# Kernel optimization log

Hardware: AMD Instinct MI355X
Metric: run time of the kernel (lower is better)

## Reference

```python
import jax, jax.numpy as jnp
import numpy as np

B, N, D = 8, 2048, 512
S = 4096  # max_swaps


def setup_inputs() -> dict:
    key = jax.random.key(0)
    ks = jax.random.split(key, 5)
    h = jax.random.normal(ks[0], (B, N, D), dtype=jnp.float32)
    indices = jax.random.randint(ks[1], (B, S, 4), 0, N, dtype=jnp.int64)
    # MLP params (Linear stores weight as (out,in) in torch; we keep (in,out) and matmul)
    W1 = jax.random.normal(ks[2], (4 * D, D), dtype=jnp.float32) * (1.0 / np.sqrt(4 * D))
    b1 = jnp.zeros((D,), dtype=jnp.float32)
    W2 = jax.random.normal(ks[3], (D, D // 2), dtype=jnp.float32) * (1.0 / np.sqrt(D))
    b2 = jnp.zeros((D // 2,), dtype=jnp.float32)
    W3 = jax.random.normal(ks[4], (D // 2, 1), dtype=jnp.float32) * (1.0 / np.sqrt(D // 2))
    b3 = jnp.zeros((1,), dtype=jnp.float32)
    return {"h": h, "indices": indices, "W1": W1, "b1": b1, "W2": W2, "b2": b2, "W3": W3, "b3": b3}


def reference(h, indices, W1, b1, W2, b2, W3, b3):
    # h: (B, N, D); indices: (B, S, 4) node ids per swap
    swap_emb = jnp.take_along_axis(h[:, None, :, :], indices[..., None].astype(jnp.int32),
                                   axis=2)  # broadcast-gather -> (B, S, 4, D)
    # equivalently: h[batch_idx, indices]; implemented as per-batch gather
    swap_emb = jax.vmap(lambda hb, ib: hb[ib])(h, indices)  # (B, S, 4, D)
    swap_feats = swap_emb.reshape(h.shape[0], indices.shape[1], -1)  # (B, S, 4D)
    x = jax.nn.gelu(swap_feats @ W1 + b1, approximate=False)
    x = jax.nn.gelu(x @ W2 + b2, approximate=False)
    scores = (x @ W3 + b3)[..., 0]  # (B, S)
    rates = jax.nn.softplus(scores)
    return rates
```

## Files before the change

kernel.cpp:

```cpp
#include <hip/hip_runtime.h>
#include <math.h>

#define BATCH 8
#define NNODES 2048
#define DDIM 512
#define SWAPS 4096
#define M_TOTAL (BATCH * SWAPS)
#define MD (BATCH * NNODES)
#define KD DDIM
#define ND (4 * DDIM)
#define K2 DDIM
#define N2 (DDIM / 2)

typedef __attribute__((ext_vector_type(8))) __bf16 bf16x8;
typedef __attribute__((ext_vector_type(4))) float f32x4;
typedef __attribute__((ext_vector_type(8))) unsigned short us8;
typedef unsigned short ushort_t;

__device__ __forceinline__ float gelu_exact(float x) {
    return 0.5f * x * (1.0f + erff(x * 0.70710678118654752440f));
}
__device__ __forceinline__ float softplus_f(float x) {
    return fmaxf(x, 0.0f) + log1pf(expf(-fabsf(x)));
}
__device__ __forceinline__ unsigned short f2bf(float f) {
    unsigned int u = __builtin_bit_cast(unsigned int, f);
    u += 0x7FFFu + ((u >> 16) & 1u);
    return (unsigned short)(u >> 16);
}
__device__ __forceinline__ float bf2f(unsigned short s) {
    return __builtin_bit_cast(float, (unsigned int)s << 16);
}
__device__ __forceinline__ void glds16(const void* g, void* l) {
    __builtin_amdgcn_global_load_lds(
        (const __attribute__((address_space(1))) void*)g,
        (__attribute__((address_space(3))) void*)l, 16, 0, 0);
}

__global__ __launch_bounds__(256) void convert_kernel(
    const float* __restrict__ h, const float* __restrict__ W1,
    const float* __restrict__ W2, ushort_t* __restrict__ h_bf,
    ushort_t* __restrict__ W1pt, ushort_t* __restrict__ W2t)
{
    const int bid = blockIdx.x;
    if (bid < 8192) {
        size_t i = ((size_t)bid * 256 + threadIdx.x) * 4;
        float4 v = *(const float4*)(h + i);
        ushort4 o = { f2bf(v.x), f2bf(v.y), f2bf(v.z), f2bf(v.w) };
        *(ushort4*)(h_bf + i) = o;
    } else if (bid < 8192 + 1024) {
        size_t e = ((size_t)(bid - 8192) * 256 + threadIdx.x) * 4;
        const int k = (int)(e >> 9), n = (int)(e & 511);
        const int sg = k >> 9, d = k & 511;
        const int j = sg * 512 + n;
        float4 v = *(const float4*)(W1 + e);
        W1pt[(size_t)(j + 0) * KD + d] = f2bf(v.x);
        W1pt[(size_t)(j + 1) * KD + d] = f2bf(v.y);
        W1pt[(size_t)(j + 2) * KD + d] = f2bf(v.z);
        W1pt[(size_t)(j + 3) * KD + d] = f2bf(v.w);
    } else {
        size_t e = ((size_t)(bid - 9216) * 256 + threadIdx.x) * 4;
        const int k = (int)(e >> 8), n = (int)(e & 255);
        float4 v = *(const float4*)(W2 + e);
        W2t[(size_t)(n + 0) * K2 + k] = f2bf(v.x);
        W2t[(size_t)(n + 1) * K2 + k] = f2bf(v.y);
        W2t[(size_t)(n + 2) * K2 + k] = f2bf(v.z);
        W2t[(size_t)(n + 3) * K2 + k] = f2bf(v.w);
    }
}

__global__ __launch_bounds__(256) void gemm1_dense(
    const ushort_t* __restrict__ h_bf, const ushort_t* __restrict__ W1pt,
    ushort_t* __restrict__ P)
{
    __shared__ __align__(16) char smem[16384];

    const int tid = threadIdx.x;
    const int w = tid >> 6, lane = tid & 63;
    const int quad = lane >> 4, l16 = lane & 15;
    const int wr = w >> 1, wc = w & 1;

    const int bid = blockIdx.x;
    const int xcd = bid & 7;
    const int r = bid >> 3;
    const int m0 = xcd * NNODES + (r & 15) * 128;
    const int n0 = (r >> 4) * 128;

    const int row0 = tid >> 2, sub = tid & 3;
    const int cg = (sub - (row0 >> 1)) & 3;
    const ushort_t* bA0 = h_bf + (size_t)(m0 + row0) * KD + cg * 8;
    const ushort_t* bA1 = h_bf + (size_t)(m0 + row0 + 64) * KD + cg * 8;
    const ushort_t* bB0 = W1pt + (size_t)(n0 + row0) * KD + cg * 8;
    const ushort_t* bB1 = W1pt + (size_t)(n0 + row0 + 64) * KD + cg * 8;

    char* ldsA0 = smem + w * 1024;
    char* ldsA1 = smem + 4096 + w * 1024;
    char* ldsB0 = smem + 8192 + w * 1024;
    char* ldsB1 = smem + 12288 + w * 1024;

    int pa[4], pb[4];
    #pragma unroll
    for (int i = 0; i < 4; ++i) {
        const int rA = wr * 64 + i * 16 + l16;
        const int rB = wc * 64 + i * 16 + l16;
        pa[i] = rA * 64 + (((quad + (rA >> 1)) & 3) * 16);
        pb[i] = 8192 + rB * 64 + (((quad + (rB >> 1)) & 3) * 16);
    }

    f32x4 acc[4][4] = {};

    for (int kt = 0; kt < 16; ++kt) {
        const int oo = kt * 32;
        glds16(bA0 + oo, ldsA0);
        glds16(bA1 + oo, ldsA1);
        glds16(bB0 + oo, ldsB0);
        glds16(bB1 + oo, ldsB1);
        __syncthreads();
        bf16x8 af[4], bfr[4];
        #pragma unroll
        for (int i = 0; i < 4; ++i) {
            af[i]  = *(const bf16x8*)(smem + pa[i]);
            bfr[i] = *(const bf16x8*)(smem + pb[i]);
        }
        #pragma unroll
        for (int i = 0; i < 4; ++i)
            #pragma unroll
            for (int jj = 0; jj < 4; ++jj)
                acc[i][jj] = __builtin_amdgcn_mfma_f32_16x16x32_bf16(
                    af[i], bfr[jj], acc[i][jj], 0, 0, 0);
        __syncthreads();
    }

    #pragma unroll
    for (int jj = 0; jj < 4; ++jj) {
        const int n = n0 + wc * 64 + jj * 16 + l16;
        #pragma unroll
        for (int i = 0; i < 4; ++i) {
            f32x4 v = acc[i][jj];
            #pragma unroll
            for (int rr = 0; rr < 4; ++rr) {
                const int m = m0 + wr * 64 + i * 16 + quad * 4 + rr;
                P[(size_t)m * ND + n] = f2bf(v[rr]);
            }
        }
    }
}

__global__ __launch_bounds__(256) void gather_sum_kernel(
    const ushort_t* __restrict__ P, const int* __restrict__ idx,
    const float* __restrict__ b1, ushort_t* __restrict__ x1_bf)
{
    const int wave = threadIdx.x >> 6, lane = threadIdx.x & 63;
    const int m = blockIdx.x * 4 + wave;
    const int b = m >> 12;
    const int4 iv = *(const int4*)(idx + (size_t)m * 4);
    const ushort_t* Pb = P + (size_t)b * NNODES * ND;
    const int n = lane * 8;

    float s[8];
    {
        float4 ba = *(const float4*)(b1 + n);
        float4 bb = *(const float4*)(b1 + n + 4);
        s[0] = ba.x; s[1] = ba.y; s[2] = ba.z; s[3] = ba.w;
        s[4] = bb.x; s[5] = bb.y; s[6] = bb.z; s[7] = bb.w;
    }
    const int nodes[4] = { iv.x, iv.y, iv.z, iv.w };
    #pragma unroll
    for (int sg = 0; sg < 4; ++sg) {
        us8 v = *(const us8*)(Pb + (size_t)nodes[sg] * ND + sg * 512 + n);
        #pragma unroll
        for (int t = 0; t < 8; ++t) s[t] += bf2f(v[t]);
    }
    ushort4 o0 = { f2bf(gelu_exact(s[0])), f2bf(gelu_exact(s[1])),
                   f2bf(gelu_exact(s[2])), f2bf(gelu_exact(s[3])) };
    ushort4 o1 = { f2bf(gelu_exact(s[4])), f2bf(gelu_exact(s[5])),
                   f2bf(gelu_exact(s[6])), f2bf(gelu_exact(s[7])) };
    *(ushort4*)(x1_bf + (size_t)m * K2 + n) = o0;
    *(ushort4*)(x1_bf + (size_t)m * K2 + n + 4) = o1;
}

__global__ __launch_bounds__(256) void gemm2_mfma(
    const ushort_t* __restrict__ x1_bf, const ushort_t* __restrict__ W2t,
    const float* __restrict__ b2, float* __restrict__ x2)
{
    __shared__ __align__(16) char smem[16384];

    const int tid = threadIdx.x;
    const int w = tid >> 6, lane = tid & 63;
    const int quad = lane >> 4, l16 = lane & 15;
    const int wr = w >> 1, wc = w & 1;
    const int m0 = blockIdx.y * 128, n0 = blockIdx.x * 128;

    const int row0 = tid >> 2, sub = tid & 3;
    const int cg = (sub - (row0 >> 1)) & 3;
    const ushort_t* bA0 = x1_bf + (size_t)(m0 + row0) * K2 + cg * 8;
    const ushort_t* bA1 = x1_bf + (size_t)(m0 + row0 + 64) * K2 + cg * 8;
    const ushort_t* bB0 = W2t + (size_t)(n0 + row0) * K2 + cg * 8;
    const ushort_t* bB1 = W2t + (size_t)(n0 + row0 + 64) * K2 + cg * 8;

    char* ldsA0 = smem + w * 1024;
    char* ldsA1 = smem + 4096 + w * 1024;
    char* ldsB0 = smem + 8192 + w * 1024;
    char* ldsB1 = smem + 12288 + w * 1024;

    int pa[4], pb[4];
    #pragma unroll
    for (int i = 0; i < 4; ++i) {
        const int rA = wr * 64 + i * 16 + l16;
        const int rB = wc * 64 + i * 16 + l16;
        pa[i] = rA * 64 + (((quad + (rA >> 1)) & 3) * 16);
        pb[i] = 8192 + rB * 64 + (((quad + (rB >> 1)) & 3) * 16);
    }

    f32x4 acc[4][4] = {};

    for (int kt = 0; kt < 16; ++kt) {
        const int oo = kt * 32;
        glds16(bA0 + oo, ldsA0);
        glds16(bA1 + oo, ldsA1);
        glds16(bB0 + oo, ldsB0);
        glds16(bB1 + oo, ldsB1);
        __syncthreads();
        bf16x8 af[4], bfr[4];
        #pragma unroll
        for (int i = 0; i < 4; ++i) {
            af[i]  = *(const bf16x8*)(smem + pa[i]);
            bfr[i] = *(const bf16x8*)(smem + pb[i]);
        }
        #pragma unroll
        for (int i = 0; i < 4; ++i)
            #pragma unroll
            for (int jj = 0; jj < 4; ++jj)
                acc[i][jj] = __builtin_amdgcn_mfma_f32_16x16x32_bf16(
                    af[i], bfr[jj], acc[i][jj], 0, 0, 0);
        __syncthreads();
    }

    #pragma unroll
    for (int jj = 0; jj < 4; ++jj) {
        const int n = n0 + wc * 64 + jj * 16 + l16;
        const float bias = b2[n];
        #pragma unroll
        for (int i = 0; i < 4; ++i) {
            f32x4 v = acc[i][jj];
            #pragma unroll
            for (int rr = 0; rr < 4; ++rr) {
                const int m = m0 + wr * 64 + i * 16 + quad * 4 + rr;
                x2[(size_t)m * N2 + n] = gelu_exact(v[rr] + bias);
            }
        }
    }
}

__global__ __launch_bounds__(256) void head_kernel(
    const float* __restrict__ x2, const float* __restrict__ W3,
    const float* __restrict__ b3, float* __restrict__ out)
{
    const int wave = threadIdx.x >> 6;
    const int lane = threadIdx.x & 63;
    const int m = blockIdx.x * 4 + wave;
    if (m >= M_TOTAL) return;

    const float* row = x2 + (size_t)m * N2;
    float s = 0.0f;
    #pragma unroll
    for (int k = 0; k < N2; k += 64) s = fmaf(row[k + lane], W3[k + lane], s);
    #pragma unroll
    for (int off = 32; off > 0; off >>= 1) s += __shfl_down(s, off);
    if (lane == 0) out[m] = softplus_f(s + b3[0]);
}

extern "C" void kernel_launch(void* const* d_in, const int* in_sizes, int n_in,
                              void* d_out, int out_size, void* d_ws, size_t ws_size,
                              hipStream_t stream) {
    const float* h   = (const float*)d_in[0];
    const int*   idx = (const int*)d_in[1];
    const float* W1  = (const float*)d_in[2];
    const float* b1  = (const float*)d_in[3];
    const float* W2  = (const float*)d_in[4];
    const float* b2  = (const float*)d_in[5];
    const float* W3  = (const float*)d_in[6];
    const float* b3  = (const float*)d_in[7];
    float* out = (float*)d_out;

    char* ws = (char*)d_ws;
    ushort_t* P     = (ushort_t*)ws;
    float*    x2    = (float*)ws;
    ushort_t* h_bf  = (ushort_t*)(ws + (64u << 20));
    ushort_t* W1pt  = (ushort_t*)(ws + (80u << 20));
    ushort_t* x1_bf = (ushort_t*)(ws + (64u << 20));
    ushort_t* W2t   = (ushort_t*)(ws + (96u << 20));

    convert_kernel<<<9344, 256, 0, stream>>>(h, W1, W2, h_bf, W1pt, W2t);
    gemm1_dense<<<2048, 256, 0, stream>>>(h_bf, W1pt, P);
    gather_sum_kernel<<<M_TOTAL / 4, 256, 0, stream>>>(P, idx, b1, x1_bf);
    gemm2_mfma<<<dim3(N2 / 128, M_TOTAL / 128), 256, 0, stream>>>(x1_bf, W2t, b2, x2);
    head_kernel<<<M_TOTAL / 4, 256, 0, stream>>>(x2, W3, b3, out);
}
```

Before: 199.4 us.

## Fuse W3 head dot-product into GEMM2 epilogue with partial row sums

Instead of writing the full GELU'd x2 matrix (32768x256 fp32) to global memory and re-reading it in a separate head kernel, the GEMM2 epilogue now multiplies each GELU output by W3, reduces across lanes with shuffles and across the two column-waves through LDS, and writes one partial sum per row per N-block. A tiny finalize kernel adds the two partials, applies the bias and softplus. This removes about 32MB of global write plus read, at the cost of extra shuffle and LDS reduction work in the epilogue and a summation order that differs slightly from before.

```diff
diff --git a/kernel.cpp b/kernel.cpp
--- a/kernel.cpp
+++ b/kernel.cpp
@@ -179,9 +179,10 @@
     *(ushort4*)(x1_bf + (size_t)m * K2 + n + 4) = o1;
 }
 
-__global__ __launch_bounds__(256) void gemm2_mfma(
+__global__ __launch_bounds__(256) void gemm2_partial(
     const ushort_t* __restrict__ x1_bf, const ushort_t* __restrict__ W2t,
-    const float* __restrict__ b2, float* __restrict__ x2)
+    const float* __restrict__ b2, const float* __restrict__ W3,
+    float* __restrict__ pp)
 {
     __shared__ __align__(16) char smem[16384];
 
@@ -236,38 +237,63 @@
         __syncthreads();
     }
 
+    float w3r[4], b2r[4];
     #pragma unroll
     for (int jj = 0; jj < 4; ++jj) {
         const int n = n0 + wc * 64 + jj * 16 + l16;
-        const float bias = b2[n];
-        #pragma unroll
-        for (int i = 0; i < 4; ++i) {
+        w3r[jj] = W3[n];
+        b2r[jj] = b2[n];
+    }
+    float part[4][4];
+    #pragma unroll
+    for (int i = 0; i < 4; ++i)
+        #pragma unroll
+        for (int rr = 0; rr < 4; ++rr) part[i][rr] = 0.0f;
+    #pragma unroll
+    for (int i = 0; i < 4; ++i)
+        #pragma unroll
+        for (int jj = 0; jj < 4; ++jj) {
             f32x4 v = acc[i][jj];
             #pragma unroll
+            for (int rr = 0; rr < 4; ++rr)
+                part[i][rr] = fmaf(gelu_exact(v[rr] + b2r[jj]), w3r[jj], part[i][rr]);
+        }
+    #pragma unroll
+    for (int off = 1; off < 16; off <<= 1)
+        #pragma unroll
+        for (int i = 0; i < 4; ++i)
+            #pragma unroll
+            for (int rr = 0; rr < 4; ++rr)
+                part[i][rr] += __shfl_xor(part[i][rr], off);
+
+    float* red = (float*)smem;
+    __syncthreads();
+    if (wc == 1 && l16 == 0) {
+        #pragma unroll
+        for (int i = 0; i < 4; ++i)
+            #pragma unroll
+            for (int rr = 0; rr < 4; ++rr)
+                red[wr * 64 + i * 16 + quad * 4 + rr] = part[i][rr];
+    }
+    __syncthreads();
+    if (wc == 0 && l16 == 0) {
+        float* dst = pp + (size_t)blockIdx.x * M_TOTAL + m0;
+        #pragma unroll
+        for (int i = 0; i < 4; ++i)
+            #pragma unroll
             for (int rr = 0; rr < 4; ++rr) {
-                const int m = m0 + wr * 64 + i * 16 + quad * 4 + rr;
-                x2[(size_t)m * N2 + n] = gelu_exact(v[rr] + bias);
+                const int r2 = wr * 64 + i * 16 + quad * 4 + rr;
+                dst[r2] = part[i][rr] + red[r2];
             }
-        }
-    }
-}
-
-__global__ __launch_bounds__(256) void head_kernel(
-    const float* __restrict__ x2, const float* __restrict__ W3,
-    const float* __restrict__ b3, float* __restrict__ out)
-{
-    const int wave = threadIdx.x >> 6;
-    const int lane = threadIdx.x & 63;
-    const int m = blockIdx.x * 4 + wave;
-    if (m >= M_TOTAL) return;
-
-    const float* row = x2 + (size_t)m * N2;
-    float s = 0.0f;
-    #pragma unroll
-    for (int k = 0; k < N2; k += 64) s = fmaf(row[k + lane], W3[k + lane], s);
-    #pragma unroll
-    for (int off = 32; off > 0; off >>= 1) s += __shfl_down(s, off);
-    if (lane == 0) out[m] = softplus_f(s + b3[0]);
+    }
+}
+
+__global__ __launch_bounds__(256) void finalize_head(
+    const float* __restrict__ pp, const float* __restrict__ b3,
+    float* __restrict__ out)
+{
+    const int m = blockIdx.x * 256 + threadIdx.x;
+    out[m] = softplus_f(pp[m] + pp[M_TOTAL + m] + b3[0]);
 }
 
 extern "C" void kernel_launch(void* const* d_in, const int* in_sizes, int n_in,
@@ -285,7 +311,7 @@
 
     char* ws = (char*)d_ws;
     ushort_t* P     = (ushort_t*)ws;
-    float*    x2    = (float*)ws;
+    float*    pp    = (float*)ws;
     ushort_t* h_bf  = (ushort_t*)(ws + (64u << 20));
     ushort_t* W1pt  = (ushort_t*)(ws + (80u << 20));
     ushort_t* x1_bf = (ushort_t*)(ws + (64u << 20));
@@ -294,6 +320,6 @@
     convert_kernel<<<9344, 256, 0, stream>>>(h, W1, W2, h_bf, W1pt, W2t);
     gemm1_dense<<<2048, 256, 0, stream>>>(h_bf, W1pt, P);
     gather_sum_kernel<<<M_TOTAL / 4, 256, 0, stream>>>(P, idx, b1, x1_bf);
-    gemm2_mfma<<<dim3(N2 / 128, M_TOTAL / 128), 256, 0, stream>>>(x1_bf, W2t, b2, x2);
-    head_kernel<<<M_TOTAL / 4, 256, 0, stream>>>(x2, W3, b3, out);
-}
+    gemm2_partial<<<dim3(N2 / 128, M_TOTAL / 128), 256, 0, stream>>>(x1_bf, W2t, b2, W3, pp);
+    finalize_head<<<M_TOTAL / 256, 256, 0, stream>>>(pp, b3, out);
+}
```

Measured after the change: 203.9 us. +2.3%, slower.
